# Optimization experiments

Hardware: AMD Instinct MI355X
Metric: run time of the kernel (lower is better)

## Reference

```python
import jax, jax.numpy as jnp
import numpy as np

EMBED_DIM = 1024
NUM_HEADS = 16
HEAD_DIM = EMBED_DIM // NUM_HEADS
B, S = 2, 2048


def setup_inputs() -> dict:
    key = jax.random.key(0)
    ks = jax.random.split(key, 9)
    scale = 1.0 / np.sqrt(EMBED_DIM)
    return {
        "x": jax.random.normal(ks[0], (B, S, EMBED_DIM), dtype=jnp.float32),
        "Wq": jax.random.normal(ks[1], (EMBED_DIM, EMBED_DIM), dtype=jnp.float32) * scale,
        "bq": jnp.zeros((EMBED_DIM,), dtype=jnp.float32),
        "Wk": jax.random.normal(ks[2], (EMBED_DIM, EMBED_DIM), dtype=jnp.float32) * scale,
        "bk": jnp.zeros((EMBED_DIM,), dtype=jnp.float32),
        "Wv": jax.random.normal(ks[3], (EMBED_DIM, EMBED_DIM), dtype=jnp.float32) * scale,
        "bv": jnp.zeros((EMBED_DIM,), dtype=jnp.float32),
        "Wo": jax.random.normal(ks[4], (EMBED_DIM, EMBED_DIM), dtype=jnp.float32) * scale,
        "bo": jnp.zeros((EMBED_DIM,), dtype=jnp.float32),
    }


def _split_heads(t):
    # [B, S, E] -> [B, H, S, Dh]
    b, s, _ = t.shape
    return t.reshape(b, s, NUM_HEADS, HEAD_DIM).transpose(0, 2, 1, 3)


def reference(x, Wq, bq, Wk, bk, Wv, bv, Wo, bo):
    q = _split_heads(x @ Wq + bq)
    k = _split_heads(x @ Wk + bk)
    v = _split_heads(x @ Wv + bv)
    scale = jnp.sqrt(jnp.asarray(HEAD_DIM, dtype=x.dtype))
    scores = jnp.einsum("bhqd,bhkd->bhqk", q, k) / scale
    attn = jax.nn.softmax(scores, axis=-1)
    out = jnp.einsum("bhqk,bhkd->bhqd", attn, v)  # [B,H,S,Dh]
    out = out.transpose(0, 2, 1, 3).reshape(x.shape[0], x.shape[1], EMBED_DIM)
    return out @ Wo + bo
```

## Files before the change

kernel.cpp:

```cpp
#include <hip/hip_runtime.h>
#include <math.h>
#include <stdint.h>

typedef __bf16 bf16;
typedef __bf16 bf16x2 __attribute__((ext_vector_type(2)));
typedef __bf16 bf16x4 __attribute__((ext_vector_type(4)));
typedef __bf16 bf16x8 __attribute__((ext_vector_type(8)));
typedef float f32x4 __attribute__((ext_vector_type(4)));
typedef float f32x16 __attribute__((ext_vector_type(16)));

constexpr int E = 1024;
constexpr int S = 2048;
constexpr int H = 16;


__device__ __forceinline__ void gload16(const void* g, void* l) {
  __builtin_amdgcn_global_load_lds(
      (__attribute__((address_space(1))) void*)(uintptr_t)g,
      (__attribute__((address_space(3))) void*)(uint32_t)(uintptr_t)l, 16, 0, 0);
}

__device__ __forceinline__ f32x4 mfma16(bf16x8 a, bf16x8 b, f32x4 c) {
  return __builtin_amdgcn_mfma_f32_16x16x32_bf16(a, b, c, 0, 0, 0);
}
__device__ __forceinline__ f32x16 mfma32(bf16x8 a, bf16x8 b, f32x16 c) {
  return __builtin_amdgcn_mfma_f32_32x32x16_bf16(a, b, c, 0, 0, 0);
}

__device__ __forceinline__ float fexp2(float x) {
#if __has_builtin(__builtin_amdgcn_exp2f)
  return __builtin_amdgcn_exp2f(x);
#else
  float r;
  asm("v_exp_f32 %0, %1" : "=v"(r) : "v"(x));
  return r;
#endif
}

__device__ __forceinline__ uint32_t pkbf(float lo, float hi) {
  bf16x2 p;
  p[0] = (bf16)lo;
  p[1] = (bf16)hi;
  return __builtin_bit_cast(uint32_t, p);
}

__global__ __launch_bounds__(256) void cast_x(const float* __restrict__ x,
                                              bf16* __restrict__ o) {
  const size_t i = ((size_t)blockIdx.x * 256 + threadIdx.x) * 8;
  const float4 a = *(const float4*)(x + i);
  const float4 b = *(const float4*)(x + i + 4);
  bf16x8 r;
  r[0] = (bf16)a.x; r[1] = (bf16)a.y; r[2] = (bf16)a.z; r[3] = (bf16)a.w;
  r[4] = (bf16)b.x; r[5] = (bf16)b.y; r[6] = (bf16)b.z; r[7] = (bf16)b.w;
  *(bf16x8*)(o + i) = r;
}

__global__ __launch_bounds__(256) void transpose_cast_w(
    const float* __restrict__ W0, const float* __restrict__ W1,
    const float* __restrict__ W2, const float* __restrict__ W3,
    bf16* __restrict__ T0, bf16* __restrict__ T1, bf16* __restrict__ T2,
    bf16* __restrict__ T3) {
  const float* W;
  bf16* T;
  switch (blockIdx.z) {
    case 0: W = W0; T = T0; break;
    case 1: W = W1; T = T1; break;
    case 2: W = W2; T = T2; break;
    default: W = W3; T = T3; break;
  }
  __shared__ float t[64][65];
  const int k0 = blockIdx.y * 64, n0 = blockIdx.x * 64;
  const int tr = threadIdx.x >> 4;
  const int tc = (threadIdx.x & 15) * 4;
#pragma unroll
  for (int u = 0; u < 4; ++u) {
    const float4 v = *(const float4*)(W + (size_t)(k0 + tr + u * 16) * E + n0 + tc);
    t[tr + u * 16][tc + 0] = v.x;
    t[tr + u * 16][tc + 1] = v.y;
    t[tr + u * 16][tc + 2] = v.z;
    t[tr + u * 16][tc + 3] = v.w;
  }
  __syncthreads();
#pragma unroll
  for (int u = 0; u < 4; ++u) {
    const int n = tr + u * 16;
    bf16x4 o;
#pragma unroll
    for (int i = 0; i < 4; ++i) o[i] = (bf16)t[tc + i][n];
    *(bf16x4*)(T + (size_t)(n0 + n) * E + k0 + tc) = o;
  }
}

__global__ __launch_bounds__(256) void gemm_qkv(const bf16* __restrict__ A,
                                                const bf16* __restrict__ Wt,
                                                const float* __restrict__ bq,
                                                const float* __restrict__ bk,
                                                const float* __restrict__ bv,
                                                bf16* __restrict__ qo,
                                                bf16* __restrict__ ko,
                                                bf16* __restrict__ vo) {
  __shared__ __attribute__((aligned(16))) bf16 Asm[128 * 32];
  __shared__ __attribute__((aligned(16))) bf16 Bsm[128 * 32];
  const int z = blockIdx.z;
  const bf16* Bt = Wt + (size_t)z * E * E;
  const float* bias = (z == 0) ? bq : (z == 1) ? bk : bv;
  const int tid = threadIdx.x;
  const int w = tid >> 6, lane = tid & 63, quad = lane >> 4, ln = lane & 15;
  const int bm = blockIdx.y * 128, bn = blockIdx.x * 128;
  const int wr = w >> 1, wc = w & 1;
  const int srow = w * 32 + (lane >> 2);
  const int scol = (lane & 3) * 8;
  const bf16* Ag = A + (size_t)(bm + srow) * E + scol;
  const bf16* Bg = Bt + (size_t)(bn + srow) * E + scol;
  f32x4 acc[4][4] = {};

  for (int k0 = 0; k0 < E; k0 += 32) {
    gload16(Ag + k0, &Asm[(w * 32) * 32]);
    gload16(Ag + k0 + (size_t)16 * E, &Asm[(w * 32 + 16) * 32]);
    gload16(Bg + k0, &Bsm[(w * 32) * 32]);
    gload16(Bg + k0 + (size_t)16 * E, &Bsm[(w * 32 + 16) * 32]);
    __syncthreads();
    bf16x8 af[4], bfr[4];
#pragma unroll
    for (int t = 0; t < 4; ++t) {
      af[t] = *(const bf16x8*)&Asm[(wr * 64 + t * 16 + ln) * 32 + quad * 8];
      bfr[t] = *(const bf16x8*)&Bsm[(wc * 64 + t * 16 + ln) * 32 + quad * 8];
    }
#pragma unroll
    for (int rt = 0; rt < 4; ++rt)
#pragma unroll
      for (int ct = 0; ct < 4; ++ct)
        acc[rt][ct] = mfma16(af[rt], bfr[ct], acc[rt][ct]);
    __syncthreads();
  }

  const float scl = (z == 0) ? 0.18033688f : 1.0f;
  const int hglob = (bn + wc * 64) >> 6;
  float bvv[4];
#pragma unroll
  for (int ct = 0; ct < 4; ++ct) bvv[ct] = bias[bn + wc * 64 + ct * 16 + ln];

#pragma unroll
  for (int rt = 0; rt < 4; ++rt) {
    const int row0 = bm + wr * 64 + rt * 16 + quad * 4;
    const int bb = row0 >> 11;
    const int rl = row0 & 2047;
    const size_t hb = (size_t)(bb * 16 + hglob) * 131072;
#pragma unroll
    for (int ct = 0; ct < 4; ++ct) {
      if (z == 2) {
        const int mt = ct >> 1, ln32 = ((ct & 1) << 4) | ln;
        const int tau = rl >> 6, hfv = (rl >> 3) & 1, j0 = rl & 7;
        bf16x4 p;
#pragma unroll
        for (int r = 0; r < 4; ++r) p[r] = (bf16)(acc[rt][ct][r] + bvv[ct]);
        *(bf16x4*)&vo[hb + (size_t)((tau * 8 + mt * 4 + rt) * 512 +
                                    hfv * 256 + ln32 * 8 + j0)] = p;
      } else {
        bf16* o = (z == 0) ? qo : ko;
        const int t = rl >> 5, ln0 = rl & 31;
        const size_t base =
            hb + (size_t)((t * 4 + ct) * 512 + (ln >> 3) * 256 + (ln & 7));
#pragma unroll
        for (int r = 0; r < 4; ++r)
          o[base + (ln0 + r) * 8] = (bf16)((acc[rt][ct][r] + bvv[ct]) * scl);
      }
    }
  }
}

__global__ __launch_bounds__(256) void gemm_wo(const bf16* __restrict__ A,
                                               const bf16* __restrict__ Bt,
                                               const float* __restrict__ bias,
                                               float* __restrict__ C) {
  __shared__ __attribute__((aligned(16))) bf16 Asm[64 * 32];
  __shared__ __attribute__((aligned(16))) bf16 Bsm[128 * 32];
  const int tid = threadIdx.x;
  const int w = tid >> 6, lane = tid & 63, quad = lane >> 4, ln = lane & 15;
  const int bm = blockIdx.y * 64, bn = blockIdx.x * 128;
  const int wr = w >> 1, wc = w & 1;
  const int sr = lane >> 2, sc = (lane & 3) * 8;
  const bf16* Ag = A + (size_t)(bm + w * 16 + sr) * E + sc;
  const bf16* Bg = Bt + (size_t)(bn + w * 32 + sr) * E + sc;
  f32x4 acc[2][4] = {};

  for (int k0 = 0; k0 < E; k0 += 32) {
    gload16(Ag + k0, &Asm[(w * 16) * 32]);
    gload16(Bg + k0, &Bsm[(w * 32) * 32]);
    gload16(Bg + k0 + (size_t)16 * E, &Bsm[(w * 32 + 16) * 32]);
    __syncthreads();
    bf16x8 af[2], bfr[4];
#pragma unroll
    for (int t = 0; t < 2; ++t)
      af[t] = *(const bf16x8*)&Asm[(wr * 32 + t * 16 + ln) * 32 + quad * 8];
#pragma unroll
    for (int t = 0; t < 4; ++t)
      bfr[t] = *(const bf16x8*)&Bsm[(wc * 64 + t * 16 + ln) * 32 + quad * 8];
#pragma unroll
    for (int rt = 0; rt < 2; ++rt)
#pragma unroll
      for (int ct = 0; ct < 4; ++ct)
        acc[rt][ct] = mfma16(af[rt], bfr[ct], acc[rt][ct]);
    __syncthreads();
  }

  float bvv[4];
#pragma unroll
  for (int ct = 0; ct < 4; ++ct) bvv[ct] = bias[bn + wc * 64 + ct * 16 + ln];
#pragma unroll
  for (int rt = 0; rt < 2; ++rt) {
    const int row0 = bm + wr * 32 + rt * 16 + quad * 4;
#pragma unroll
    for (int ct = 0; ct < 4; ++ct) {
      const int c = bn + wc * 64 + ct * 16 + ln;
#pragma unroll
      for (int r = 0; r < 4; ++r)
        C[(size_t)(row0 + r) * E + c] = acc[rt][ct][r] + bvv[ct];
    }
  }
}

__global__ __launch_bounds__(256, 2) void attn_mfma(const bf16* __restrict__ Qf,
                                                    const bf16* __restrict__ Kf,
                                                    const bf16* __restrict__ Vf,
                                                    bf16* __restrict__ Og) {
  __shared__ __attribute__((aligned(16))) char smem[65536];

  const int tid = threadIdx.x;
  const int w = tid >> 6, lane = tid & 63, ln = lane & 31, hf = lane >> 5;
  const int qi = w & 1, ki = w >> 1;
  const int q64 = blockIdx.x * 2 + qi;
  const int h = blockIdx.y, b = blockIdx.z;
  const size_t fb = (size_t)(b * H + h) * 131072;

  bf16x8 qf[2][4];
#pragma unroll
  for (int qg = 0; qg < 2; ++qg) {
    const bf16* qb = Qf + fb + (size_t)(q64 * 2 + qg) * 2048 + lane * 8;
#pragma unroll
    for (int c = 0; c < 4; ++c) qf[qg][c] = *(const bf16x8*)(qb + c * 512);
  }

  const bf16* Ksrc = Kf + fb + qi * 2048 + lane * 8;
  const bf16* Vsrc = Vf + fb + qi * 2048 + lane * 8;
  const int dstoff = ki * 4096 + qi * 2048;

  float lpart[2] = {0.f, 0.f};
  f32x16 oacc[2][2] = {};

#define STAGE(i, buf)                                                   \
  do {                                                                  \
    const size_t toff = (size_t)(ki * 16 + (i)) * 4096;                 \
    bf16* kd = (bf16*)(smem + (buf) * 32768) + dstoff;                  \
    bf16* vd = (bf16*)(smem + (buf) * 32768 + 16384) + dstoff;          \
    _Pragma("unroll") for (int c = 0; c < 4; ++c) {                     \
      gload16(Ksrc + toff + c * 512, kd + c * 512);                     \
      gload16(Vsrc + toff + c * 512, vd + c * 512);                     \
    }                                                                   \
  } while (0)

  STAGE(0, 0);
  __syncthreads();

#pragma unroll 2
  for (int i = 0; i < 16; ++i) {
    const int cur = i & 1;
    if (i < 15) STAGE(i + 1, cur ^ 1);
    const bf16* Ks = (const bf16*)(smem + cur * 32768) + ki * 4096;
    const bf16* Vs = (const bf16*)(smem + cur * 32768 + 16384) + ki * 4096;

#pragma unroll
    for (int mt = 0; mt < 2; ++mt) {
      bf16x8 kf4[4];
#pragma unroll
      for (int c = 0; c < 4; ++c)
        kf4[c] = *(const bf16x8*)&Ks[(mt * 4 + c) * 512 + lane * 8];

      f32x16 st[2] = {{}, {}};
      __builtin_amdgcn_s_setprio(1);
#pragma unroll
      for (int c = 0; c < 4; ++c) {
        st[0] = mfma32(kf4[c], qf[0][c], st[0]);
        st[1] = mfma32(kf4[c], qf[1][c], st[1]);
      }
      __builtin_amdgcn_s_setprio(0);

      bf16x8 pb[2][2];
#pragma unroll
      for (int qg = 0; qg < 2; ++qg) {
        float pe[16];
#pragma unroll
        for (int r = 0; r < 16; ++r) {
          pe[r] = fexp2(st[qg][r]);
          lpart[qg] += pe[r];
        }
#pragma unroll
        for (int cl = 0; cl < 2; ++cl) {
          uint32_t a01 = pkbf(pe[cl * 8 + 0], pe[cl * 8 + 1]);
          uint32_t a23 = pkbf(pe[cl * 8 + 2], pe[cl * 8 + 3]);
          uint32_t b01 = pkbf(pe[cl * 8 + 4], pe[cl * 8 + 5]);
          uint32_t b23 = pkbf(pe[cl * 8 + 6], pe[cl * 8 + 7]);
          auto r0 = __builtin_amdgcn_permlane32_swap(a01, b01, false, false);
          auto r1 = __builtin_amdgcn_permlane32_swap(a23, b23, false, false);
          union {
            bf16x8 v;
            uint32_t u[4];
          } pu;
          pu.u[0] = r0[0];
          pu.u[1] = r1[0];
          pu.u[2] = r0[1];
          pu.u[3] = r1[1];
          pb[qg][cl] = pu.v;
        }
      }

      bf16x8 vf[2][2];
#pragma unroll
      for (int vt = 0; vt < 2; ++vt)
#pragma unroll
        for (int cl = 0; cl < 2; ++cl)
          vf[vt][cl] =
              *(const bf16x8*)&Vs[(vt * 4 + mt * 2 + cl) * 512 + lane * 8];

      __builtin_amdgcn_s_setprio(1);
#pragma unroll
      for (int qg = 0; qg < 2; ++qg)
#pragma unroll
        for (int vt = 0; vt < 2; ++vt) {
          oacc[qg][vt] = mfma32(vf[vt][0], pb[qg][0], oacc[qg][vt]);
          oacc[qg][vt] = mfma32(vf[vt][1], pb[qg][1], oacc[qg][vt]);
        }
      __builtin_amdgcn_s_setprio(0);
    }
    __syncthreads();
  }
#undef STAGE

  float* Ocmb = (float*)smem;
  float* Lcmb = (float*)(smem + 32768);
  if (ki == 1) {
#pragma unroll
    for (int qg = 0; qg < 2; ++qg) {
#pragma unroll
      for (int vt = 0; vt < 2; ++vt)
#pragma unroll
        for (int r = 0; r < 16; ++r)
          Ocmb[(qi * 2 + qg) * 2048 + (vt * 16 + r) * 64 + lane] =
              oacc[qg][vt][r];
      Lcmb[(qi * 2 + qg) * 64 + lane] = lpart[qg];
    }
  }
  __syncthreads();
  if (ki == 0) {
#pragma unroll
    for (int qg = 0; qg < 2; ++qg) {
#pragma unroll
      for (int vt = 0; vt < 2; ++vt)
#pragma unroll
        for (int r = 0; r < 16; ++r)
          oacc[qg][vt][r] +=
              Ocmb[(qi * 2 + qg) * 2048 + (vt * 16 + r) * 64 + lane];
      float lp = lpart[qg] + Lcmb[(qi * 2 + qg) * 64 + lane];

      lp += __shfl_xor(lp, 32);
      const float inv = 1.0f / lp;

      bf16* orow =
          Og + ((size_t)b * S + (size_t)q64 * 64 + qg * 32 + ln) * E + h * 64;
#pragma unroll
      for (int vt = 0; vt < 2; ++vt) {
#pragma unroll
        for (int g = 0; g < 4; ++g) {
          bf16x4 o;
#pragma unroll
          for (int j = 0; j < 4; ++j)
            o[j] = (bf16)(oacc[qg][vt][g * 4 + j] * inv);
          *(bf16x4*)&orow[vt * 32 + g * 8 + hf * 4] = o;
        }
      }
    }
  }
}

extern "C" void kernel_launch(void* const* d_in, const int* in_sizes, int n_in,
                              void* d_out, int out_size, void* d_ws, size_t ws_size,
                              hipStream_t stream) {
  const float* x = (const float*)d_in[0];
  const float* Wq = (const float*)d_in[1];
  const float* bq = (const float*)d_in[2];
  const float* Wk = (const float*)d_in[3];
  const float* bk = (const float*)d_in[4];
  const float* Wv = (const float*)d_in[5];
  const float* bv = (const float*)d_in[6];
  const float* Wo = (const float*)d_in[7];
  const float* bo = (const float*)d_in[8];

  const size_t ME = (size_t)4096 * 1024;
  const size_t WE = (size_t)1024 * 1024;
  bf16* xb = (bf16*)d_ws;
  bf16* wqt = xb + ME;
  bf16* wkt = wqt + WE;
  bf16* wvt = wkt + WE;
  bf16* wot = wvt + WE;
  bf16* qb = wot + WE;
  bf16* kb = qb + ME;
  bf16* vt = kb + ME;
  bf16* ab = vt + ME;

  cast_x<<<2048, 256, 0, stream>>>(x, xb);
  transpose_cast_w<<<dim3(16, 16, 4), 256, 0, stream>>>(Wq, Wk, Wv, Wo, wqt, wkt,
                                                        wvt, wot);
  gemm_qkv<<<dim3(8, 32, 3), 256, 0, stream>>>(xb, wqt, bq, bk, bv, qb, kb, vt);
  attn_mfma<<<dim3(S / 128, H, 2), 256, 0, stream>>>(qb, kb, vt, ab);
  gemm_wo<<<dim3(8, 64), 256, 0, stream>>>(ab, wot, bo, (float*)d_out);
}
```

Baseline: 186.8 us.

## Split attention KV range across four wave groups with 512-thread blocks

The attention kernel grows from 256 to 512 threads per block, so four KV-split wave groups each handle a quarter of the keys, with a smaller per-iteration tile (one 32-key slice instead of two). Partial outputs and row sums are merged through a two-level shared-memory reduction. This is meant to give more waves per CU to hide latency and to shorten the serial loop per wave. The cost is extra reduction passes and barriers, more LDS per block (about 66 KB), and higher register pressure under launch_bounds(512,4). The row-sum accumulation also becomes a tree sum instead of a serial one.

Result: slower. 269.4 us (+44.2%).

```diff
diff --git a/kernel.cpp b/kernel.cpp
--- a/kernel.cpp
+++ b/kernel.cpp
@@ -220,43 +220,45 @@
   }
 }
 
-__global__ __launch_bounds__(256, 2) void attn_mfma(const bf16* __restrict__ Qf,
-                                                    const bf16* __restrict__ Kf,
-                                                    const bf16* __restrict__ Vf,
-                                                    bf16* __restrict__ Og) {
-  __shared__ __attribute__((aligned(16))) char smem[65536];
+__global__ __launch_bounds__(512, 4) void attn_mfma(
+    const bf16* __restrict__ Qf, const bf16* __restrict__ Kf,
+    const bf16* __restrict__ Vf, bf16* __restrict__ Og) {
+  __shared__ __attribute__((aligned(16))) char smem[67584];
 
   const int tid = threadIdx.x;
   const int w = tid >> 6, lane = tid & 63, ln = lane & 31, hf = lane >> 5;
   const int qi = w & 1, ki = w >> 1;
-  const int q64 = blockIdx.x * 2 + qi;
   const int h = blockIdx.y, b = blockIdx.z;
   const size_t fb = (size_t)(b * H + h) * 131072;
 
   bf16x8 qf[2][4];
 #pragma unroll
   for (int qg = 0; qg < 2; ++qg) {
-    const bf16* qb = Qf + fb + (size_t)(q64 * 2 + qg) * 2048 + lane * 8;
+    const bf16* qb =
+        Qf + fb + (size_t)(blockIdx.x * 4 + qi * 2 + qg) * 2048 + lane * 8;
 #pragma unroll
     for (int c = 0; c < 4; ++c) qf[qg][c] = *(const bf16x8*)(qb + c * 512);
   }
 
-  const bf16* Ksrc = Kf + fb + qi * 2048 + lane * 8;
-  const bf16* Vsrc = Vf + fb + qi * 2048 + lane * 8;
-  const int dstoff = ki * 4096 + qi * 2048;
+  const bf16* Ksrc = Kf + fb + lane * 8;
+  const bf16* Vsrc = Vf + fb + lane * 8;
 
   float lpart[2] = {0.f, 0.f};
   f32x16 oacc[2][2] = {};
 
-#define STAGE(i, buf)                                                   \
-  do {                                                                  \
-    const size_t toff = (size_t)(ki * 16 + (i)) * 4096;                 \
-    bf16* kd = (bf16*)(smem + (buf) * 32768) + dstoff;                  \
-    bf16* vd = (bf16*)(smem + (buf) * 32768 + 16384) + dstoff;          \
-    _Pragma("unroll") for (int c = 0; c < 4; ++c) {                     \
-      gload16(Ksrc + toff + c * 512, kd + c * 512);                     \
-      gload16(Vsrc + toff + c * 512, vd + c * 512);                     \
-    }                                                                   \
+#define STAGE(i, buf)                                                       \
+  do {                                                                      \
+    const int t = ki * 16 + (i);                                            \
+    const int tau = t >> 1, p = (i) & 1;                                    \
+    bf16* base = (bf16*)smem + (buf) * 16384;                               \
+    gload16(Ksrc + (size_t)t * 2048 + (qi * 2 + 0) * 512,                   \
+            base + ki * 2048 + (qi * 2 + 0) * 512);                         \
+    gload16(Ksrc + (size_t)t * 2048 + (qi * 2 + 1) * 512,                   \
+            base + ki * 2048 + (qi * 2 + 1) * 512);                         \
+    gload16(Vsrc + (size_t)(tau * 8 + qi * 4 + p * 2 + 0) * 512,            \
+            base + 8192 + ki * 2048 + qi * 1024 + 0 * 512);                 \
+    gload16(Vsrc + (size_t)(tau * 8 + qi * 4 + p * 2 + 1) * 512,            \
+            base + 8192 + ki * 2048 + qi * 1024 + 1 * 512);                 \
   } while (0)
 
   STAGE(0, 0);
@@ -266,107 +268,134 @@
   for (int i = 0; i < 16; ++i) {
     const int cur = i & 1;
     if (i < 15) STAGE(i + 1, cur ^ 1);
-    const bf16* Ks = (const bf16*)(smem + cur * 32768) + ki * 4096;
-    const bf16* Vs = (const bf16*)(smem + cur * 32768 + 16384) + ki * 4096;
-
-#pragma unroll
-    for (int mt = 0; mt < 2; ++mt) {
-      bf16x8 kf4[4];
-#pragma unroll
-      for (int c = 0; c < 4; ++c)
-        kf4[c] = *(const bf16x8*)&Ks[(mt * 4 + c) * 512 + lane * 8];
-
-      f32x16 st[2] = {{}, {}};
-      __builtin_amdgcn_s_setprio(1);
-#pragma unroll
-      for (int c = 0; c < 4; ++c) {
-        st[0] = mfma32(kf4[c], qf[0][c], st[0]);
-        st[1] = mfma32(kf4[c], qf[1][c], st[1]);
+    const bf16* Kc = (const bf16*)smem + cur * 16384 + ki * 2048;
+    const bf16* Vc = (const bf16*)smem + cur * 16384 + 8192 + ki * 2048;
+
+    bf16x8 kf4[4];
+#pragma unroll
+    for (int c = 0; c < 4; ++c)
+      kf4[c] = *(const bf16x8*)&Kc[c * 512 + lane * 8];
+
+    f32x16 st[2] = {{}, {}};
+    __builtin_amdgcn_s_setprio(1);
+#pragma unroll
+    for (int c = 0; c < 4; ++c) {
+      st[0] = mfma32(kf4[c], qf[0][c], st[0]);
+      st[1] = mfma32(kf4[c], qf[1][c], st[1]);
+    }
+    __builtin_amdgcn_s_setprio(0);
+
+    bf16x8 pb[2][2];
+#pragma unroll
+    for (int qg = 0; qg < 2; ++qg) {
+      float pe[16];
+#pragma unroll
+      for (int r = 0; r < 16; ++r) pe[r] = fexp2(st[qg][r]);
+      lpart[qg] += (((pe[0] + pe[1]) + (pe[2] + pe[3])) +
+                    ((pe[4] + pe[5]) + (pe[6] + pe[7]))) +
+                   (((pe[8] + pe[9]) + (pe[10] + pe[11])) +
+                    ((pe[12] + pe[13]) + (pe[14] + pe[15])));
+#pragma unroll
+      for (int cl = 0; cl < 2; ++cl) {
+        uint32_t a01 = pkbf(pe[cl * 8 + 0], pe[cl * 8 + 1]);
+        uint32_t a23 = pkbf(pe[cl * 8 + 2], pe[cl * 8 + 3]);
+        uint32_t b01 = pkbf(pe[cl * 8 + 4], pe[cl * 8 + 5]);
+        uint32_t b23 = pkbf(pe[cl * 8 + 6], pe[cl * 8 + 7]);
+        auto r0 = __builtin_amdgcn_permlane32_swap(a01, b01, false, false);
+        auto r1 = __builtin_amdgcn_permlane32_swap(a23, b23, false, false);
+        union {
+          bf16x8 v;
+          uint32_t u[4];
+        } pu;
+        pu.u[0] = r0[0];
+        pu.u[1] = r1[0];
+        pu.u[2] = r0[1];
+        pu.u[3] = r1[1];
+        pb[qg][cl] = pu.v;
       }
-      __builtin_amdgcn_s_setprio(0);
-
-      bf16x8 pb[2][2];
-#pragma unroll
-      for (int qg = 0; qg < 2; ++qg) {
-        float pe[16];
-#pragma unroll
-        for (int r = 0; r < 16; ++r) {
-          pe[r] = fexp2(st[qg][r]);
-          lpart[qg] += pe[r];
-        }
-#pragma unroll
-        for (int cl = 0; cl < 2; ++cl) {
-          uint32_t a01 = pkbf(pe[cl * 8 + 0], pe[cl * 8 + 1]);
-          uint32_t a23 = pkbf(pe[cl * 8 + 2], pe[cl * 8 + 3]);
-          uint32_t b01 = pkbf(pe[cl * 8 + 4], pe[cl * 8 + 5]);
-          uint32_t b23 = pkbf(pe[cl * 8 + 6], pe[cl * 8 + 7]);
-          auto r0 = __builtin_amdgcn_permlane32_swap(a01, b01, false, false);
-          auto r1 = __builtin_amdgcn_permlane32_swap(a23, b23, false, false);
-          union {
-            bf16x8 v;
-            uint32_t u[4];
-          } pu;
-          pu.u[0] = r0[0];
-          pu.u[1] = r1[0];
-          pu.u[2] = r0[1];
-          pu.u[3] = r1[1];
-          pb[qg][cl] = pu.v;
-        }
+    }
+
+    bf16x8 vf[2][2];
+#pragma unroll
+    for (int vt = 0; vt < 2; ++vt)
+#pragma unroll
+      for (int cl = 0; cl < 2; ++cl)
+        vf[vt][cl] = *(const bf16x8*)&Vc[vt * 1024 + cl * 512 + lane * 8];
+
+    __builtin_amdgcn_s_setprio(1);
+#pragma unroll
+    for (int qg = 0; qg < 2; ++qg)
+#pragma unroll
+      for (int vt = 0; vt < 2; ++vt) {
+        oacc[qg][vt] = mfma32(vf[vt][0], pb[qg][0], oacc[qg][vt]);
+        oacc[qg][vt] = mfma32(vf[vt][1], pb[qg][1], oacc[qg][vt]);
       }
-
-      bf16x8 vf[2][2];
+    __builtin_amdgcn_s_setprio(0);
+
+    __syncthreads();
+  }
+#undef STAGE
+
+  float* Oc = (float*)smem;
+  float* Lc = (float*)(smem + 65536);
+  if (ki >= 2) {
+#pragma unroll
+    for (int qg = 0; qg < 2; ++qg) {
+      const int s = (qi * 2 + qg) * 2 + (ki - 2);
 #pragma unroll
       for (int vt = 0; vt < 2; ++vt)
 #pragma unroll
-        for (int cl = 0; cl < 2; ++cl)
-          vf[vt][cl] =
-              *(const bf16x8*)&Vs[(vt * 4 + mt * 2 + cl) * 512 + lane * 8];
-
-      __builtin_amdgcn_s_setprio(1);
-#pragma unroll
-      for (int qg = 0; qg < 2; ++qg)
-#pragma unroll
-        for (int vt = 0; vt < 2; ++vt) {
-          oacc[qg][vt] = mfma32(vf[vt][0], pb[qg][0], oacc[qg][vt]);
-          oacc[qg][vt] = mfma32(vf[vt][1], pb[qg][1], oacc[qg][vt]);
-        }
-      __builtin_amdgcn_s_setprio(0);
-    }
-    __syncthreads();
-  }
-#undef STAGE
-
-  float* Ocmb = (float*)smem;
-  float* Lcmb = (float*)(smem + 32768);
+        for (int r = 0; r < 16; ++r)
+          Oc[s * 2048 + (vt * 16 + r) * 64 + lane] = oacc[qg][vt][r];
+      Lc[s * 64 + lane] = lpart[qg];
+    }
+  }
+  __syncthreads();
+  if (ki < 2) {
+#pragma unroll
+    for (int qg = 0; qg < 2; ++qg) {
+      const int s = (qi * 2 + qg) * 2 + ki;
+#pragma unroll
+      for (int vt = 0; vt < 2; ++vt)
+#pragma unroll
+        for (int r = 0; r < 16; ++r)
+          oacc[qg][vt][r] += Oc[s * 2048 + (vt * 16 + r) * 64 + lane];
+      lpart[qg] += Lc[s * 64 + lane];
+    }
+  }
+  __syncthreads();
   if (ki == 1) {
 #pragma unroll
     for (int qg = 0; qg < 2; ++qg) {
+      const int s = (qi * 2 + qg) * 2;
 #pragma unroll
       for (int vt = 0; vt < 2; ++vt)
 #pragma unroll
         for (int r = 0; r < 16; ++r)
-          Ocmb[(qi * 2 + qg) * 2048 + (vt * 16 + r) * 64 + lane] =
-              oacc[qg][vt][r];
-      Lcmb[(qi * 2 + qg) * 64 + lane] = lpart[qg];
+          Oc[s * 2048 + (vt * 16 + r) * 64 + lane] = oacc[qg][vt][r];
+      Lc[s * 64 + lane] = lpart[qg];
     }
   }
   __syncthreads();
   if (ki == 0) {
 #pragma unroll
     for (int qg = 0; qg < 2; ++qg) {
+      const int s = (qi * 2 + qg) * 2;
 #pragma unroll
       for (int vt = 0; vt < 2; ++vt)
 #pragma unroll
         for (int r = 0; r < 16; ++r)
-          oacc[qg][vt][r] +=
-              Ocmb[(qi * 2 + qg) * 2048 + (vt * 16 + r) * 64 + lane];
-      float lp = lpart[qg] + Lcmb[(qi * 2 + qg) * 64 + lane];
+          oacc[qg][vt][r] += Oc[s * 2048 + (vt * 16 + r) * 64 + lane];
+      float lp = lpart[qg] + Lc[s * 64 + lane];
 
       lp += __shfl_xor(lp, 32);
       const float inv = 1.0f / lp;
 
       bf16* orow =
-          Og + ((size_t)b * S + (size_t)q64 * 64 + qg * 32 + ln) * E + h * 64;
+          Og +
+          ((size_t)b * S + (size_t)(blockIdx.x * 4 + qi * 2 + qg) * 32 + ln) *
+              E +
+          h * 64;
 #pragma unroll
       for (int vt = 0; vt < 2; ++vt) {
 #pragma unroll
@@ -411,6 +440,6 @@
   transpose_cast_w<<<dim3(16, 16, 4), 256, 0, stream>>>(Wq, Wk, Wv, Wo, wqt, wkt,
                                                         wvt, wot);
   gemm_qkv<<<dim3(8, 32, 3), 256, 0, stream>>>(xb, wqt, bq, bk, bv, qb, kb, vt);
-  attn_mfma<<<dim3(S / 128, H, 2), 256, 0, stream>>>(qb, kb, vt, ab);
+  attn_mfma<<<dim3(S / 128, H, 2), 512, 0, stream>>>(qb, kb, vt, ab);
   gemm_wo<<<dim3(8, 64), 256, 0, stream>>>(ab, wot, bo, (float*)d_out);
 }
```
